# Kernel optimization log

Measured on AMD Instinct MI355X. Metric: run time of the kernel, lower is better.

## Reference

```python
import jax, jax.numpy as jnp
import numpy as np

EPS_LN = 1e-5
EPS_ACT = 1e-5
EPS_W = 1e-8


def _layer_norm(x):
    # F.layer_norm(x, [d]) with no affine params, eps=1e-5, biased variance
    mu = jnp.mean(x, axis=-1, keepdims=True)
    xc = x - mu
    var = jnp.mean(xc * xc, axis=-1, keepdims=True)
    return xc * jax.lax.rsqrt(var + EPS_LN)


def _activation_quant(x):
    # per-token absmax int8 fake-quant (dequantized back to float)
    scale = 127.0 / jnp.clip(jnp.max(jnp.abs(x), axis=-1, keepdims=True), EPS_ACT)
    return jnp.clip(jnp.round(x * scale), -128, 127) / scale


def _weight_quant(w):
    # ternary {-1,0,+1} absmean quantization, rescaled by absmean
    scale = jnp.clip(jnp.mean(jnp.abs(w)), EPS_W)
    return jnp.clip(jnp.round(w / scale), -1, 1) * scale


def _bitlinear(x, w, b):
    xn = _layer_norm(x)
    xq = _activation_quant(xn)        # forward value (STE irrelevant for fwd)
    wq = _weight_quant(w)
    return jnp.einsum('bsd,fd->bsf', xq, wq) + b


def setup_inputs() -> dict:
    key = jax.random.key(0)
    k1, k2, k3, k4, k5 = jax.random.split(key, 5)
    d_model, d_ff = 2048, 8192
    B, S = 4, 2048
    x = jax.random.normal(k1, (B, S, d_model), dtype=jnp.float32)
    # nn.Linear default init: U(-1/sqrt(fan_in), 1/sqrt(fan_in))
    lim1 = 1.0 / np.sqrt(d_model)
    lim2 = 1.0 / np.sqrt(d_ff)
    w1 = jax.random.uniform(k2, (d_ff, d_model), jnp.float32, -lim1, lim1)
    b1 = jax.random.uniform(k3, (d_ff,), jnp.float32, -lim1, lim1)
    w2 = jax.random.uniform(k4, (d_model, d_ff), jnp.float32, -lim2, lim2)
    b2 = jax.random.uniform(k5, (d_model,), jnp.float32, -lim2, lim2)
    return {"x": x, "w1": w1, "b1": b1, "w2": w2, "b2": b2}


def reference(x, w1, b1, w2, b2):
    h = _bitlinear(x, w1, b1)
    h = jax.nn.gelu(h, approximate=False)  # torch F.gelu default = exact erf
    # dropout p=0.0 -> identity
    return _bitlinear(h, w2, b2)
```

## Files before the change

### kernel.cpp

```cpp
#include <hip/hip_runtime.h>

typedef int      i32x4  __attribute__((ext_vector_type(4)));
typedef int      i32x16 __attribute__((ext_vector_type(16)));
typedef _Float16 f16x2  __attribute__((ext_vector_type(2)));

__device__ __forceinline__ void async_cp16(const void* g, void* l) {
    __builtin_amdgcn_global_load_lds(
        (const __attribute__((address_space(1))) void*)g,
        (__attribute__((address_space(3))) void*)l, 16, 0, 0);
}

__device__ __forceinline__ void stage2(const signed char* g0, const signed char* g1,
                                       signed char* slab, int ldst) {
    async_cp16(g0, slab + ldst);
    async_cp16(g1, slab + 8192 + ldst);
}

__device__ __forceinline__ void rd_frags(const signed char* sa, const signed char* sb,
                                         int aoff0, int aoff1, int boff0, int boff1,
                                         i32x4 af[4][2], i32x4 bf[2][2]) {
#pragma unroll
    for (int mb = 0; mb < 4; ++mb) {
        af[mb][0] = *(const i32x4*)(sa + mb * 2048 + aoff0);
        af[mb][1] = *(const i32x4*)(sa + mb * 2048 + aoff1);
    }
#pragma unroll
    for (int nb = 0; nb < 2; ++nb) {
        bf[nb][0] = *(const i32x4*)(sb + nb * 2048 + boff0);
        bf[nb][1] = *(const i32x4*)(sb + nb * 2048 + boff1);
    }
}

__device__ __forceinline__ void mfma16x(const i32x4 af[4][2], const i32x4 bf[2][2],
                                        i32x16 acc[4][2]) {
#pragma unroll
    for (int ks = 0; ks < 2; ++ks)
#pragma unroll
        for (int mb = 0; mb < 4; ++mb)
#pragma unroll
            for (int nb = 0; nb < 2; ++nb)
                acc[mb][nb] = __builtin_amdgcn_mfma_i32_32x32x32_i8(
                    af[mb][ks], bf[nb][ks], acc[mb][nb], 0, 0, 0);
}

#define LGKM0 do { asm volatile("s_waitcnt lgkmcnt(0)" ::: "memory"); \
                   __builtin_amdgcn_sched_barrier(0); } while (0)
#define VMW(N) do { asm volatile("s_waitcnt vmcnt(" #N ")" ::: "memory"); \
                    __builtin_amdgcn_sched_barrier(0); } while (0)
#define GNONE do { } while (0)

template <bool GELU, typename OutT>
__global__ __launch_bounds__(512, 2) void gemm_i8_32(
    const signed char* __restrict__ A,
    const signed char* __restrict__ B,
    const float* __restrict__ rowinv,
    const float* __restrict__ wscale,
    const float* __restrict__ bias,
    OutT* __restrict__ C,
    int M, int N, int K)
{
    __shared__ signed char sA[4][16384];
    __shared__ signed char sB[4][16384];

    const int tid  = threadIdx.x;
    const int lane = tid & 63;
    const int wid  = tid >> 6;
    const int wm   = wid >> 2;
    const int wn   = wid & 3;

    const int nwg = gridDim.x * gridDim.y;
    const int bid = blockIdx.y * gridDim.x + blockIdx.x;
    const int cpx = nwg >> 3;
    const int wg  = (bid & 7) * cpx + (bid >> 3);
    const int bx  = wg % gridDim.x;
    const int by  = wg / gridDim.x;

    const long long rowA0 = (long long)by * 256;
    const long long rowB0 = (long long)bx * 256;

    const int srow   = tid >> 2;
    const int schunk = (tid & 3) ^ ((tid >> 3) & 3);
    const signed char* aG0 = A + (rowA0 + srow) * (long long)K + schunk * 16;
    const signed char* aG1 = aG0 + 128LL * K;
    const signed char* bG0 = B + (rowB0 + srow) * (long long)K + schunk * 16;
    const signed char* bG1 = bG0 + 128LL * K;
    const int ldst = tid * 16;

    const int r32 = lane & 31;
    const int kc  = lane >> 5;
    const int swz = (r32 >> 1) & 3;
    const int sl0 = ((0 * 2 + kc) ^ swz) << 4;
    const int sl1 = ((1 * 2 + kc) ^ swz) << 4;
    const int aoff0 = wm * 8192 + r32 * 64 + sl0;
    const int aoff1 = wm * 8192 + r32 * 64 + sl1;
    const int boff0 = wn * 4096 + r32 * 64 + sl0;
    const int boff1 = wn * 4096 + r32 * 64 + sl1;

    const int NTt = K >> 7;

    i32x16 acc[4][2] = {};
    i32x4 af[4][2], bf[2][2];

#define PH(SL, DOST, KOFF, GATE) do {                                          \
        rd_frags(sA[SL], sB[SL], aoff0, aoff1, boff0, boff1, af, bf);          \
        if (DOST) {                                                            \
            stage2(aG0 + (KOFF), aG1 + (KOFF), sA[(SL + 3) & 3], ldst);        \
            stage2(bG0 + (KOFF), bG1 + (KOFF), sB[(SL + 3) & 3], ldst);        \
        }                                                                      \
        __builtin_amdgcn_s_barrier(); LGKM0;                                   \
        __builtin_amdgcn_s_setprio(1); mfma16x(af, bf, acc);                   \
        __builtin_amdgcn_s_setprio(0);                                         \
        GATE; __builtin_amdgcn_s_barrier();                                    \
    } while (0)

    stage2(aG0,       aG1,       sA[0], ldst); stage2(bG0,       bG1,       sB[0], ldst);
    stage2(aG0 + 64,  aG1 + 64,  sA[1], ldst); stage2(bG0 + 64,  bG1 + 64,  sB[1], ldst);
    stage2(aG0 + 128, aG1 + 128, sA[2], ldst); stage2(bG0 + 128, bG1 + 128, sB[2], ldst);
    VMW(8); __builtin_amdgcn_s_barrier();

    int koff = 192;
    for (int t = 0; t < NTt - 2; t += 2) {
        PH(0, true, koff,       VMW(8));
        PH(1, true, koff + 64,  VMW(8));
        PH(2, true, koff + 128, VMW(8));
        PH(3, true, koff + 192, VMW(8));
        koff += 256;
    }
    PH(0, true,  koff, VMW(8));
    PH(1, false, 0,    VMW(4));
    PH(2, false, 0,    VMW(0));
    PH(3, false, 0,    GNONE);
#undef PH

    const float sw = wscale[0];
    float bjv[2];
#pragma unroll
    for (int nb = 0; nb < 2; ++nb)
        bjv[nb] = bias[rowB0 + wn * 64 + nb * 32 + r32];
#pragma unroll
    for (int mb = 0; mb < 4; ++mb) {
#pragma unroll
        for (int r = 0; r < 16; ++r) {
            const int lrow = (r & 3) + 8 * (r >> 2) + 4 * kc;
            const long long gr = rowA0 + wm * 128 + mb * 32 + lrow;
            const float rs = sw * rowinv[gr];
#pragma unroll
            for (int nb = 0; nb < 2; ++nb) {
                const long long gc = rowB0 + wn * 64 + nb * 32 + r32;
                float v = (float)acc[mb][nb][r] * rs + bjv[nb];
                if constexpr (GELU)
                    v = 0.5f * v * (1.0f + erff(v * 0.70710678118654752f));
                C[gr * (long long)N + gc] = (OutT)v;
            }
        }
    }
}

__global__ __launch_bounds__(256) void ln_quant_x(
    const float* __restrict__ x, signed char* __restrict__ xq,
    float* __restrict__ xinv)
{
    const int t = blockIdx.x;
    const int tid = threadIdx.x;
    const int lane = tid & 63, wid = tid >> 6;
    const float4* row = (const float4*)(x + (long long)t * 2048);
    float4 v0 = row[tid];
    float4 v1 = row[tid + 256];
    float vv[8] = {v0.x, v0.y, v0.z, v0.w, v1.x, v1.y, v1.z, v1.w};

    float s = 0.f, mn = vv[0], mx = vv[0];
#pragma unroll
    for (int i = 0; i < 8; ++i) { s += vv[i]; mn = fminf(mn, vv[i]); mx = fmaxf(mx, vv[i]); }
#pragma unroll
    for (int off = 32; off > 0; off >>= 1) {
        s += __shfl_down(s, off);
        mn = fminf(mn, __shfl_down(mn, off));
        mx = fmaxf(mx, __shfl_down(mx, off));
    }
    __shared__ float rS[4], rMn[4], rMx[4];
    if (lane == 0) { rS[wid] = s; rMn[wid] = mn; rMx[wid] = mx; }
    __syncthreads();
    s  = rS[0] + rS[1] + rS[2] + rS[3];
    mn = fminf(fminf(rMn[0], rMn[1]), fminf(rMn[2], rMn[3]));
    mx = fmaxf(fmaxf(rMx[0], rMx[1]), fmaxf(rMx[2], rMx[3]));
    const float mu = s * (1.0f / 2048.0f);

    float ssc = 0.f;
#pragma unroll
    for (int i = 0; i < 8; ++i) { float d = vv[i] - mu; ssc += d * d; }
#pragma unroll
    for (int off = 32; off > 0; off >>= 1) ssc += __shfl_down(ssc, off);
    __syncthreads();
    if (lane == 0) rS[wid] = ssc;
    __syncthreads();
    ssc = rS[0] + rS[1] + rS[2] + rS[3];

    const float var  = ssc * (1.0f / 2048.0f);
    const float rstd = 1.0f / sqrtf(var + 1e-5f);
    float am = fmaxf(mx - mu, mu - mn) * rstd;
    am = fmaxf(am, 1e-5f);
    const float scale = 127.0f / am;

    unsigned int b0 = 0, b1 = 0;
#pragma unroll
    for (int i = 0; i < 8; ++i) {
        float xn = (vv[i] - mu) * rstd;
        int qi = (int)fminf(fmaxf(rintf(xn * scale), -128.0f), 127.0f);
        unsigned int byte = (unsigned int)(qi & 0xff);
        if (i < 4) b0 |= byte << (i * 8);
        else       b1 |= byte << ((i - 4) * 8);
    }
    int* orow = (int*)(xq + (long long)t * 2048);
    orow[tid]       = (int)b0;
    orow[tid + 256] = (int)b1;
    if (tid == 0) xinv[t] = am / 127.0f;
}

__global__ __launch_bounds__(256) void ln_quant_h(
    const unsigned short* __restrict__ h, signed char* __restrict__ hq,
    float* __restrict__ hinv)
{
    const long long t = blockIdx.x;
    const int tid = threadIdx.x;
    const int lane = tid & 63, wid = tid >> 6;
    const unsigned short* row = h + t * 8192;

    uint4 raw[4];
    float v[32];
#pragma unroll
    for (int c = 0; c < 4; ++c) raw[c] = ((const uint4*)row)[c * 256 + tid];
#pragma unroll
    for (int c = 0; c < 4; ++c) {
        unsigned int u[4] = {raw[c].x, raw[c].y, raw[c].z, raw[c].w};
#pragma unroll
        for (int k = 0; k < 4; ++k) {
            f16x2 p = __builtin_bit_cast(f16x2, u[k]);
            v[c * 8 + k * 2 + 0] = (float)p[0];
            v[c * 8 + k * 2 + 1] = (float)p[1];
        }
    }

    float s = 0.f, mn = v[0], mx = v[0];
#pragma unroll
    for (int i = 0; i < 32; ++i) { s += v[i]; mn = fminf(mn, v[i]); mx = fmaxf(mx, v[i]); }
#pragma unroll
    for (int off = 32; off > 0; off >>= 1) {
        s += __shfl_down(s, off);
        mn = fminf(mn, __shfl_down(mn, off));
        mx = fmaxf(mx, __shfl_down(mx, off));
    }
    __shared__ float rS[4], rMn[4], rMx[4];
    if (lane == 0) { rS[wid] = s; rMn[wid] = mn; rMx[wid] = mx; }
    __syncthreads();
    s  = rS[0] + rS[1] + rS[2] + rS[3];
    mn = fminf(fminf(rMn[0], rMn[1]), fminf(rMn[2], rMn[3]));
    mx = fmaxf(fmaxf(rMx[0], rMx[1]), fmaxf(rMx[2], rMx[3]));
    const float mu = s * (1.0f / 8192.0f);

    float ssc = 0.f;
#pragma unroll
    for (int i = 0; i < 32; ++i) { float d = v[i] - mu; ssc += d * d; }
#pragma unroll
    for (int off = 32; off > 0; off >>= 1) ssc += __shfl_down(ssc, off);
    __syncthreads();
    if (lane == 0) rS[wid] = ssc;
    __syncthreads();
    ssc = rS[0] + rS[1] + rS[2] + rS[3];

    const float var  = ssc * (1.0f / 8192.0f);
    const float rstd = 1.0f / sqrtf(var + 1e-5f);
    float am = fmaxf(mx - mu, mu - mn) * rstd;
    am = fmaxf(am, 1e-5f);
    const float scale = 127.0f / am;

    signed char* orow = hq + t * 8192;
#pragma unroll
    for (int c = 0; c < 4; ++c) {
        unsigned int b0 = 0, b1 = 0;
#pragma unroll
        for (int k = 0; k < 8; ++k) {
            float xn = (v[c * 8 + k] - mu) * rstd;
            int qi = (int)fminf(fmaxf(rintf(xn * scale), -128.0f), 127.0f);
            unsigned int byte = (unsigned int)(qi & 0xff);
            if (k < 4) b0 |= byte << (k * 8);
            else       b1 |= byte << ((k - 4) * 8);
        }
        int2 o; o.x = (int)b0; o.y = (int)b1;
        ((int2*)orow)[c * 256 + tid] = o;
    }
    if (tid == 0) hinv[t] = am / 127.0f;
}

__global__ __launch_bounds__(256) void reduce_abs(
    const float4* __restrict__ w4, int n4, float* __restrict__ partial)
{
    const int tid = threadIdx.x;
    const int lane = tid & 63, wid = tid >> 6;
    float s = 0.f;
    for (int i = blockIdx.x * 256 + tid; i < n4; i += gridDim.x * 256) {
        float4 v = w4[i];
        s += fabsf(v.x) + fabsf(v.y) + fabsf(v.z) + fabsf(v.w);
    }
#pragma unroll
    for (int off = 32; off > 0; off >>= 1) s += __shfl_down(s, off);
    __shared__ float rS[4];
    if (lane == 0) rS[wid] = s;
    __syncthreads();
    if (tid == 0) partial[blockIdx.x] = rS[0] + rS[1] + rS[2] + rS[3];
}

__global__ __launch_bounds__(256) void finalize_scales(
    const float* __restrict__ p1, const float* __restrict__ p2,
    float* __restrict__ scales)
{
    const int tid = threadIdx.x;
    const int lane = tid & 63, wid = tid >> 6;
    float s1 = 0.f, s2 = 0.f;
    for (int i = tid; i < 1024; i += 256) { s1 += p1[i]; s2 += p2[i]; }
#pragma unroll
    for (int off = 32; off > 0; off >>= 1) {
        s1 += __shfl_down(s1, off);
        s2 += __shfl_down(s2, off);
    }
    __shared__ float rA[4], rB[4];
    if (lane == 0) { rA[wid] = s1; rB[wid] = s2; }
    __syncthreads();
    if (tid == 0) {
        float m1 = fmaxf((rA[0] + rA[1] + rA[2] + rA[3]) * (1.0f / 16777216.0f), 1e-8f);
        float m2 = fmaxf((rB[0] + rB[1] + rB[2] + rB[3]) * (1.0f / 16777216.0f), 1e-8f);
        scales[0] = m1;
        scales[1] = m2;
    }
}

__global__ __launch_bounds__(256) void quant_w(
    const float4* __restrict__ w4, signed char* __restrict__ wq,
    const float* __restrict__ scales, int sidx, int n4)
{
    const float s = scales[sidx];
    for (int i = blockIdx.x * 256 + threadIdx.x; i < n4; i += gridDim.x * 256) {
        float4 v = w4[i];
        int q0 = (int)fminf(fmaxf(rintf(v.x / s), -1.0f), 1.0f);
        int q1 = (int)fminf(fmaxf(rintf(v.y / s), -1.0f), 1.0f);
        int q2 = (int)fminf(fmaxf(rintf(v.z / s), -1.0f), 1.0f);
        int q3 = (int)fminf(fmaxf(rintf(v.w / s), -1.0f), 1.0f);
        unsigned int p = (unsigned int)(q0 & 0xff) | ((unsigned int)(q1 & 0xff) << 8)
                       | ((unsigned int)(q2 & 0xff) << 16) | ((unsigned int)(q3 & 0xff) << 24);
        ((unsigned int*)wq)[i] = p;
    }
}

extern "C" void kernel_launch(void* const* d_in, const int* in_sizes, int n_in,
                              void* d_out, int out_size, void* d_ws, size_t ws_size,
                              hipStream_t stream)
{
    const float* x  = (const float*)d_in[0];
    const float* w1 = (const float*)d_in[1];
    const float* b1 = (const float*)d_in[2];
    const float* w2 = (const float*)d_in[3];
    const float* b2 = (const float*)d_in[4];
    float* out = (float*)d_out;

    char* ws = (char*)d_ws;
    const size_t SZ_WQ = 16777216;
    signed char* w1q = (signed char*)(ws);
    signed char* w2q = (signed char*)(ws + SZ_WQ);
    signed char* xq  = (signed char*)(ws + 2 * SZ_WQ);
    unsigned short* h = (unsigned short*)(ws + 3 * SZ_WQ);
    signed char* hq  = (signed char*)(ws + 3 * SZ_WQ + 134217728);
    float* xinv   = (float*)(ws + 3 * SZ_WQ + 134217728 + 67108864);
    float* hinv   = xinv + 8192;
    float* part1  = hinv + 8192;
    float* part2  = part1 + 1024;
    float* scales = part2 + 1024;

    const int N4W = 4194304;

    reduce_abs<<<1024, 256, 0, stream>>>((const float4*)w1, N4W, part1);
    reduce_abs<<<1024, 256, 0, stream>>>((const float4*)w2, N4W, part2);
    finalize_scales<<<1, 256, 0, stream>>>(part1, part2, scales);
    quant_w<<<4096, 256, 0, stream>>>((const float4*)w1, w1q, scales, 0, N4W);
    quant_w<<<4096, 256, 0, stream>>>((const float4*)w2, w2q, scales, 1, N4W);
    ln_quant_x<<<8192, 256, 0, stream>>>(x, xq, xinv);

    gemm_i8_32<true, _Float16><<<dim3(32, 32), 512, 0, stream>>>(
        xq, w1q, xinv, &scales[0], b1, (_Float16*)h, 8192, 8192, 2048);

    ln_quant_h<<<8192, 256, 0, stream>>>(h, hq, hinv);

    gemm_i8_32<false, float><<<dim3(8, 32), 512, 0, stream>>>(
        hq, w2q, hinv, &scales[1], b2, out, 8192, 2048, 8192);
}
```

Baseline: 619.5 us.

## Overlap LDS fragment reads with MFMA via double-buffered registers and 8-way swizzle

Restructures the int8 GEMM main loop so that each 64-wide K stage is split into two half-steps with ping-pong register fragments. The next half's LDS reads are issued while the current half's MFMAs run. It also removes one barrier per stage and changes the LDS layout to an 8-chunk XOR swizzle with two rows packed per 128-byte line, aiming to cut bank conflicts. The cost is more live registers for the second fragment set and a more delicate wait/barrier ordering in the 4-slot ring buffer.

```diff
diff --git a/kernel.cpp b/kernel.cpp
--- a/kernel.cpp
+++ b/kernel.cpp
@@ -16,41 +16,14 @@
     async_cp16(g1, slab + 8192 + ldst);
 }
 
-__device__ __forceinline__ void rd_frags(const signed char* sa, const signed char* sb,
-                                         int aoff0, int aoff1, int boff0, int boff1,
-                                         i32x4 af[4][2], i32x4 bf[2][2]) {
-#pragma unroll
-    for (int mb = 0; mb < 4; ++mb) {
-        af[mb][0] = *(const i32x4*)(sa + mb * 2048 + aoff0);
-        af[mb][1] = *(const i32x4*)(sa + mb * 2048 + aoff1);
-    }
-#pragma unroll
-    for (int nb = 0; nb < 2; ++nb) {
-        bf[nb][0] = *(const i32x4*)(sb + nb * 2048 + boff0);
-        bf[nb][1] = *(const i32x4*)(sb + nb * 2048 + boff1);
-    }
-}
-
-__device__ __forceinline__ void mfma16x(const i32x4 af[4][2], const i32x4 bf[2][2],
-                                        i32x16 acc[4][2]) {
-#pragma unroll
-    for (int ks = 0; ks < 2; ++ks)
-#pragma unroll
-        for (int mb = 0; mb < 4; ++mb)
-#pragma unroll
-            for (int nb = 0; nb < 2; ++nb)
-                acc[mb][nb] = __builtin_amdgcn_mfma_i32_32x32x32_i8(
-                    af[mb][ks], bf[nb][ks], acc[mb][nb], 0, 0, 0);
-}
-
-#define LGKM0 do { asm volatile("s_waitcnt lgkmcnt(0)" ::: "memory"); \
-                   __builtin_amdgcn_sched_barrier(0); } while (0)
 #define VMW(N) do { asm volatile("s_waitcnt vmcnt(" #N ")" ::: "memory"); \
                     __builtin_amdgcn_sched_barrier(0); } while (0)
-#define GNONE do { } while (0)
+#define BARX do { __builtin_amdgcn_sched_barrier(0); \
+                  __builtin_amdgcn_s_barrier(); \
+                  __builtin_amdgcn_sched_barrier(0); } while (0)
 
 template <bool GELU, typename OutT>
-__global__ __launch_bounds__(512, 2) void gemm_i8_32(
+__global__ __launch_bounds__(512, 2) void gemm_i8_ov(
     const signed char* __restrict__ A,
     const signed char* __restrict__ B,
     const float* __restrict__ rowinv,
@@ -78,61 +51,98 @@
     const long long rowA0 = (long long)by * 256;
     const long long rowB0 = (long long)bx * 256;
 
-    const int srow   = tid >> 2;
-    const int schunk = (tid & 3) ^ ((tid >> 3) & 3);
-    const signed char* aG0 = A + (rowA0 + srow) * (long long)K + schunk * 16;
+    const int cp_   = (tid & 7) ^ ((tid >> 3) & 7);
+    const int srow2 = ((tid >> 3) << 1) + (cp_ >> 2);
+    const int sk16  = (cp_ & 3) << 4;
+    const signed char* aG0 = A + (rowA0 + srow2) * (long long)K + sk16;
     const signed char* aG1 = aG0 + 128LL * K;
-    const signed char* bG0 = B + (rowB0 + srow) * (long long)K + schunk * 16;
+    const signed char* bG0 = B + (rowB0 + srow2) * (long long)K + sk16;
     const signed char* bG1 = bG0 + 128LL * K;
     const int ldst = tid * 16;
 
-    const int r32 = lane & 31;
-    const int kc  = lane >> 5;
-    const int swz = (r32 >> 1) & 3;
-    const int sl0 = ((0 * 2 + kc) ^ swz) << 4;
-    const int sl1 = ((1 * 2 + kc) ^ swz) << 4;
-    const int aoff0 = wm * 8192 + r32 * 64 + sl0;
-    const int aoff1 = wm * 8192 + r32 * 64 + sl1;
-    const int boff0 = wn * 4096 + r32 * 64 + sl0;
-    const int boff1 = wn * 4096 + r32 * 64 + sl1;
-
-    const int NTt = K >> 7;
+    const int r32  = lane & 31;
+    const int kc   = lane >> 5;
+    const int key  = (r32 >> 1) & 7;
+    const int rhb  = ((r32 & 1) << 2);
+    const int rowb = (r32 >> 1) * 128;
+    const int sq0  = ((rhb | (0 + kc)) ^ key) << 4;
+    const int sq1  = ((rhb | (2 + kc)) ^ key) << 4;
+    const int aoff0 = wm * 8192 + rowb + sq0;
+    const int aoff1 = wm * 8192 + rowb + sq1;
+    const int boff0 = wn * 4096 + rowb + sq0;
+    const int boff1 = wn * 4096 + rowb + sq1;
+
+    const int NP = K >> 6;
 
     i32x16 acc[4][2] = {};
-    i32x4 af[4][2], bf[2][2];
-
-#define PH(SL, DOST, KOFF, GATE) do {                                          \
-        rd_frags(sA[SL], sB[SL], aoff0, aoff1, boff0, boff1, af, bf);          \
-        if (DOST) {                                                            \
-            stage2(aG0 + (KOFF), aG1 + (KOFF), sA[(SL + 3) & 3], ldst);        \
-            stage2(bG0 + (KOFF), bG1 + (KOFF), sB[(SL + 3) & 3], ldst);        \
-        }                                                                      \
-        __builtin_amdgcn_s_barrier(); LGKM0;                                   \
-        __builtin_amdgcn_s_setprio(1); mfma16x(af, bf, acc);                   \
+    i32x4 afE[4], bfE[2], afO[4], bfO[2];
+
+#define RD6(SL, AOFF, BOFF, AF, BF) do {                                       \
+        _Pragma("unroll")                                                      \
+        for (int mb_ = 0; mb_ < 4; ++mb_)                                      \
+            AF[mb_] = *(const i32x4*)(sA[SL] + mb_ * 2048 + (AOFF));           \
+        _Pragma("unroll")                                                      \
+        for (int nb_ = 0; nb_ < 2; ++nb_)                                      \
+            BF[nb_] = *(const i32x4*)(sB[SL] + nb_ * 2048 + (BOFF));           \
+    } while (0)
+
+#define MFMA8(AF, BF) do {                                                     \
+        __builtin_amdgcn_s_setprio(1);                                         \
+        _Pragma("unroll")                                                      \
+        for (int mb_ = 0; mb_ < 4; ++mb_)                                      \
+            _Pragma("unroll")                                                  \
+            for (int nb_ = 0; nb_ < 2; ++nb_)                                  \
+                acc[mb_][nb_] = __builtin_amdgcn_mfma_i32_32x32x32_i8(         \
+                    AF[mb_], BF[nb_], acc[mb_][nb_], 0, 0, 0);                 \
         __builtin_amdgcn_s_setprio(0);                                         \
-        GATE; __builtin_amdgcn_s_barrier();                                    \
     } while (0)
 
     stage2(aG0,       aG1,       sA[0], ldst); stage2(bG0,       bG1,       sB[0], ldst);
     stage2(aG0 + 64,  aG1 + 64,  sA[1], ldst); stage2(bG0 + 64,  bG1 + 64,  sB[1], ldst);
     stage2(aG0 + 128, aG1 + 128, sA[2], ldst); stage2(bG0 + 128, bG1 + 128, sB[2], ldst);
-    VMW(8); __builtin_amdgcn_s_barrier();
-
-    int koff = 192;
-    for (int t = 0; t < NTt - 2; t += 2) {
-        PH(0, true, koff,       VMW(8));
-        PH(1, true, koff + 64,  VMW(8));
-        PH(2, true, koff + 128, VMW(8));
-        PH(3, true, koff + 192, VMW(8));
-        koff += 256;
-    }
-    PH(0, true,  koff, VMW(8));
-    PH(1, false, 0,    VMW(4));
-    PH(2, false, 0,    VMW(0));
-    PH(3, false, 0,    GNONE);
-#undef PH
-
-    const float sw = wscale[0];
+    VMW(4); BARX;
+    RD6(0, aoff0, boff0, afE, bfE);
+
+    long long koff = 192;
+    for (int p = 0; p <= NP - 4; ++p) {
+        const int s0 = p & 3, s1 = (p + 1) & 3, sw = (p + 3) & 3;
+        stage2(aG0 + koff, aG1 + koff, sA[sw], ldst);
+        stage2(bG0 + koff, bG1 + koff, sB[sw], ldst);
+        RD6(s0, aoff1, boff1, afO, bfO);
+        MFMA8(afE, bfE);
+        RD6(s1, aoff0, boff0, afE, bfE);
+        MFMA8(afO, bfO);
+        VMW(4); BARX;
+        koff += 64;
+    }
+    {
+        const int p = NP - 3;
+        const int s0 = p & 3, s1 = (p + 1) & 3;
+        RD6(s0, aoff1, boff1, afO, bfO);
+        MFMA8(afE, bfE);
+        RD6(s1, aoff0, boff0, afE, bfE);
+        MFMA8(afO, bfO);
+        VMW(0); BARX;
+    }
+    {
+        const int p = NP - 2;
+        const int s0 = p & 3, s1 = (p + 1) & 3;
+        RD6(s0, aoff1, boff1, afO, bfO);
+        MFMA8(afE, bfE);
+        RD6(s1, aoff0, boff0, afE, bfE);
+        MFMA8(afO, bfO);
+    }
+    {
+        const int p = NP - 1;
+        const int s0 = p & 3;
+        RD6(s0, aoff1, boff1, afO, bfO);
+        MFMA8(afE, bfE);
+        MFMA8(afO, bfO);
+    }
+#undef RD6
+#undef MFMA8
+
+    const float sw_ = wscale[0];
     float bjv[2];
 #pragma unroll
     for (int nb = 0; nb < 2; ++nb)
@@ -143,7 +153,7 @@
         for (int r = 0; r < 16; ++r) {
             const int lrow = (r & 3) + 8 * (r >> 2) + 4 * kc;
             const long long gr = rowA0 + wm * 128 + mb * 32 + lrow;
-            const float rs = sw * rowinv[gr];
+            const float rs = sw_ * rowinv[gr];
 #pragma unroll
             for (int nb = 0; nb < 2; ++nb) {
                 const long long gc = rowB0 + wn * 64 + nb * 32 + r32;
@@ -383,11 +393,11 @@
     quant_w<<<4096, 256, 0, stream>>>((const float4*)w2, w2q, scales, 1, N4W);
     ln_quant_x<<<8192, 256, 0, stream>>>(x, xq, xinv);
 
-    gemm_i8_32<true, _Float16><<<dim3(32, 32), 512, 0, stream>>>(
+    gemm_i8_ov<true, _Float16><<<dim3(32, 32), 512, 0, stream>>>(
         xq, w1q, xinv, &scales[0], b1, (_Float16*)h, 8192, 8192, 2048);
 
     ln_quant_h<<<8192, 256, 0, stream>>>(h, hq, hinv);
 
-    gemm_i8_32<false, float><<<dim3(8, 32), 512, 0, stream>>>(
+    gemm_i8_ov<false, float><<<dim3(8, 32), 512, 0, stream>>>(
         hq, w2q, hinv, &scales[1], b2, out, 8192, 2048, 8192);
 }
```

Result: slower. 659.4 us (+6.4%).
